# Performance work log

Hardware: AMD Instinct MI355X
Metric: run time of the kernel (lower is better)

The kernel has to match this reference:

```python
import jax, jax.numpy as jnp
import numpy as np

E, O, I = 8, 512, 1024  # num_experts, out_features, in_features
TOK_PER_EXPERT = 8192
T = E * TOK_PER_EXPERT  # total routed tokens


def setup_inputs() -> dict:
    key = jax.random.key(0)
    k1, k2 = jax.random.split(key)
    inputs = jax.random.normal(k1, (T, I), dtype=jnp.float32)
    # Learned per-expert weights, shape (E, O, I) as in GraniteMoeParallelExperts
    weight = jax.random.normal(k2, (E, O, I), dtype=jnp.float32) * (1.0 / np.sqrt(I))
    return {"inputs": inputs, "weight": weight, "expert_size": TOK_PER_EXPERT}


def reference(inputs, weight, expert_size):
    # inputs: [T, I] tokens sorted by expert; expert_size tokens per expert (static).
    # Equivalent to: split(inputs, expert_size) -> per-expert x @ W_e^T -> concat.
    e, o, i = weight.shape
    x = inputs.reshape(e, expert_size, i)          # [E, S, I]
    out = jnp.einsum('esi,eoi->eso', x, weight)    # grouped GEMM, [E, S, O]
    return out.reshape(e * expert_size, o)         # [T, O]
```

## Files before the change

kernel.cpp:

```cpp
#include <hip/hip_runtime.h>
#include <hip/hip_bf16.h>


#define NE 8
#define NO 512
#define NI 1024
#define NS 8192

#define BM 256
#define BN 256
#define BK 64
#define NT (NI / BK)

typedef __attribute__((ext_vector_type(4))) float f32x4;
typedef __attribute__((ext_vector_type(4))) short s16x4;
typedef __attribute__((ext_vector_type(8))) short s16x8;

__device__ __forceinline__ s16x4 cvt4(f32x4 a) {
    s16x4 r;
    r[0] = (short)__builtin_bit_cast(unsigned short, __float2bfloat16(a[0]));
    r[1] = (short)__builtin_bit_cast(unsigned short, __float2bfloat16(a[1]));
    r[2] = (short)__builtin_bit_cast(unsigned short, __float2bfloat16(a[2]));
    r[3] = (short)__builtin_bit_cast(unsigned short, __float2bfloat16(a[3]));
    return r;
}

__global__ __launch_bounds__(256)
void pack_w(const float* __restrict__ W, short* __restrict__ Wb) {
    size_t idx = (size_t)blockIdx.x * 256 + threadIdx.x;
    const float* src = W + idx * 8;
    f32x4 a = *(const f32x4*)src;
    f32x4 b = *(const f32x4*)(src + 4);
    s16x8 r;
    s16x4 lo = cvt4(a), hi = cvt4(b);
    r[0] = lo[0]; r[1] = lo[1]; r[2] = lo[2]; r[3] = lo[3];
    r[4] = hi[0]; r[5] = hi[1]; r[6] = hi[2]; r[7] = hi[3];
    *(s16x8*)(Wb + idx * 8) = r;
}

__global__ __launch_bounds__(512, 2)
void moe_gemm(const float* __restrict__ X,
              const short* __restrict__ Wb,
              float* __restrict__ Out) {
    int bid  = blockIdx.x;
    int swz  = (bid & 7) * 64 + (bid >> 3);
    int e    = swz >> 6;
    int rem  = swz & 63;
    int mblk = rem >> 1;
    int nblk = rem & 1;

    const float* Ap = X   + ((size_t)e * NS + (size_t)mblk * BM) * NI;
    const short* Bp = Wb  + ((size_t)e * NO + (size_t)nblk * BN) * NI;
    float*       Cp = Out + ((size_t)e * NS + (size_t)mblk * BM) * NO + nblk * BN;

    __shared__ short lA[2][BM * BK];
    __shared__ short lB[2][BN * BK];

    const int tid  = threadIdx.x;
    const int lane = tid & 63;
    const int wid  = tid >> 6;
    const int wm   = wid >> 2;
    const int wn   = wid & 3;
    const int l15  = lane & 15;
    const int lhi  = lane >> 4;

    f32x4 acc[8][4];
#pragma unroll
    for (int i = 0; i < 8; ++i)
#pragma unroll
        for (int j = 0; j < 4; ++j)
            acc[i][j] = (f32x4){0.f, 0.f, 0.f, 0.f};

    f32x4 ar[8];

#define AISSUE(kt)                                                             \
    do {                                                                       \
        _Pragma("unroll") for (int i = 0; i < 8; ++i) {                        \
            int u = tid + i * 512;                                             \
            ar[i] = *(const f32x4*)(Ap + (size_t)(u >> 4) * NI +               \
                                    (kt) * BK + (u & 15) * 4);                 \
        }                                                                      \
    } while (0)

#define AWRITE(buf)                                                            \
    do {                                                                       \
        _Pragma("unroll") for (int i = 0; i < 8; ++i) {                        \
            int u    = tid + i * 512;                                          \
            int row  = u >> 4;                                                 \
            int c4   = u & 15;                                                 \
            int phys = (c4 >> 1) ^ (row & 7);                                  \
            *(s16x4*)&lA[buf][row * 64 + phys * 8 + (c4 & 1) * 4] = cvt4(ar[i]); \
        }                                                                      \
    } while (0)

#define BSTAGE(kt, buf)                                                        \
    do {                                                                       \
        _Pragma("unroll") for (int j = 0; j < 4; ++j) {                        \
            int g    = (wid * 4 + j) * 64 + lane;                              \
            int row  = g >> 3;                                                 \
            int k16  = g & 7;                                                  \
            const short* gp = Bp + (size_t)row * NI + (kt) * BK +              \
                              ((k16 ^ (row & 7)) << 3);                        \
            short* lp = &lB[buf][(wid * 4 + j) * 512];                         \
            __builtin_amdgcn_global_load_lds(                                  \
                (const __attribute__((address_space(1))) void*)gp,             \
                (__attribute__((address_space(3))) void*)lp, 16, 0, 0);        \
        }                                                                      \
    } while (0)

#define COMPUTE(buf)                                                           \
    do {                                                                       \
        _Pragma("unroll") for (int kk = 0; kk < 2; ++kk) {                     \
            s16x8 af[8], bf_[4];                                               \
            _Pragma("unroll") for (int mi = 0; mi < 8; ++mi) {                 \
                int r    = wm * 128 + mi * 16 + l15;                           \
                int phys = (kk * 4 + lhi) ^ (r & 7);                           \
                af[mi]   = *(const s16x8*)&lA[buf][r * 64 + phys * 8];         \
            }                                                                  \
            _Pragma("unroll") for (int ni = 0; ni < 4; ++ni) {                 \
                int rb   = wn * 64 + ni * 16 + l15;                            \
                int phys = (kk * 4 + lhi) ^ (rb & 7);                          \
                bf_[ni]  = *(const s16x8*)&lB[buf][rb * 64 + phys * 8];        \
            }                                                                  \
            _Pragma("unroll") for (int mi = 0; mi < 8; ++mi)                   \
                _Pragma("unroll") for (int ni = 0; ni < 4; ++ni)               \
                    acc[mi][ni] = __builtin_amdgcn_mfma_f32_16x16x32_bf16(     \
                        af[mi], bf_[ni], acc[mi][ni], 0, 0, 0);                \
        }                                                                      \
    } while (0)

    AISSUE(0);
    BSTAGE(0, 0);

#pragma unroll 1
    for (int kt = 0; kt < NT; ++kt) {
        const int c = kt & 1;
        __builtin_amdgcn_s_barrier();
        asm volatile("s_waitcnt vmcnt(4)" ::: "memory");
        AWRITE(c);
        if (kt + 1 < NT) {
            AISSUE(kt + 1);
            BSTAGE(kt + 1, c ^ 1);
            asm volatile("s_waitcnt vmcnt(12)" ::: "memory");
        } else {
            asm volatile("s_waitcnt vmcnt(0)" ::: "memory");
        }
        asm volatile("s_waitcnt lgkmcnt(0)" ::: "memory");
        __builtin_amdgcn_s_barrier();
        COMPUTE(c);
    }

#pragma unroll
    for (int mi = 0; mi < 8; ++mi) {
#pragma unroll
        for (int rr = 0; rr < 4; ++rr) {
            int row   = wm * 128 + mi * 16 + lhi * 4 + rr;
            float* cp = Cp + (size_t)row * NO + wn * 64 + l15;
#pragma unroll
            for (int ni = 0; ni < 4; ++ni)
                cp[ni * 16] = acc[mi][ni][rr];
        }
    }
#undef AISSUE
#undef AWRITE
#undef BSTAGE
#undef COMPUTE
}

extern "C" void kernel_launch(void* const* d_in, const int* in_sizes, int n_in,
                              void* d_out, int out_size, void* d_ws, size_t ws_size,
                              hipStream_t stream) {
    const float* X = (const float*)d_in[0];
    const float* W = (const float*)d_in[1];
    float* Out     = (float*)d_out;
    short* Wb      = (short*)d_ws;

    hipLaunchKernelGGL(pack_w, dim3(2048), dim3(256), 0, stream, W, Wb);
    hipLaunchKernelGGL(moe_gemm, dim3(NE * (NS / BM) * (NO / BN)), dim3(512), 0,
                       stream, X, Wb, Out);
}
```

Baseline: 138.6 us.

## Restructure GEMM main loop into four interleaved phases with prefetch distance two

Splits each K-tile's compute into four phases of LDS reads plus MFMA, with barriers between them. The fp32 A loads and the bf16 conversion writes are spread across the phases, and A global loads are issued two tiles ahead. MFMA blocks run at raised priority via s_setprio. The occupancy hint drops to one 512-thread block per CU, giving more registers for the deeper prefetch and halved fragment arrays. The aim is to overlap global loads, LDS traffic and matrix math, at the cost of more barriers and lower occupancy.

Result: faster. 127.5 us (-8.0%).

```diff
diff --git a/kernel.cpp b/kernel.cpp
--- a/kernel.cpp
+++ b/kernel.cpp
@@ -38,7 +38,7 @@
     *(s16x8*)(Wb + idx * 8) = r;
 }
 
-__global__ __launch_bounds__(512, 2)
+__global__ __launch_bounds__(512, 1)
 void moe_gemm(const float* __restrict__ X,
               const short* __restrict__ Wb,
               float* __restrict__ Out) {
@@ -72,19 +72,20 @@
             acc[i][j] = (f32x4){0.f, 0.f, 0.f, 0.f};
 
     f32x4 ar[8];
-
-#define AISSUE(kt)                                                             \
-    do {                                                                       \
-        _Pragma("unroll") for (int i = 0; i < 8; ++i) {                        \
+    s16x8 af[4], bf_[4];
+
+#define AISSUE_H(kt, h)                                                        \
+    do {                                                                       \
+        _Pragma("unroll") for (int i = (h) * 4; i < (h) * 4 + 4; ++i) {        \
             int u = tid + i * 512;                                             \
             ar[i] = *(const f32x4*)(Ap + (size_t)(u >> 4) * NI +               \
                                     (kt) * BK + (u & 15) * 4);                 \
         }                                                                      \
     } while (0)
 
-#define AWRITE(buf)                                                            \
-    do {                                                                       \
-        _Pragma("unroll") for (int i = 0; i < 8; ++i) {                        \
+#define AWRITE_H(buf, h)                                                       \
+    do {                                                                       \
+        _Pragma("unroll") for (int i = (h) * 4; i < (h) * 4 + 4; ++i) {        \
             int u    = tid + i * 512;                                          \
             int row  = u >> 4;                                                 \
             int c4   = u & 15;                                                 \
@@ -108,46 +109,78 @@
         }                                                                      \
     } while (0)
 
-#define COMPUTE(buf)                                                           \
-    do {                                                                       \
-        _Pragma("unroll") for (int kk = 0; kk < 2; ++kk) {                     \
-            s16x8 af[8], bf_[4];                                               \
-            _Pragma("unroll") for (int mi = 0; mi < 8; ++mi) {                 \
-                int r    = wm * 128 + mi * 16 + l15;                           \
-                int phys = (kk * 4 + lhi) ^ (r & 7);                           \
-                af[mi]   = *(const s16x8*)&lA[buf][r * 64 + phys * 8];         \
-            }                                                                  \
-            _Pragma("unroll") for (int ni = 0; ni < 4; ++ni) {                 \
-                int rb   = wn * 64 + ni * 16 + l15;                            \
-                int phys = (kk * 4 + lhi) ^ (rb & 7);                          \
-                bf_[ni]  = *(const s16x8*)&lB[buf][rb * 64 + phys * 8];        \
-            }                                                                  \
-            _Pragma("unroll") for (int mi = 0; mi < 8; ++mi)                   \
-                _Pragma("unroll") for (int ni = 0; ni < 4; ++ni)               \
-                    acc[mi][ni] = __builtin_amdgcn_mfma_f32_16x16x32_bf16(     \
-                        af[mi], bf_[ni], acc[mi][ni], 0, 0, 0);                \
-        }                                                                      \
-    } while (0)
-
-    AISSUE(0);
+#define PH_READ_A(c, kk, mh)                                                   \
+    do {                                                                       \
+        _Pragma("unroll") for (int j = 0; j < 4; ++j) {                        \
+            int r    = wm * 128 + ((mh) * 4 + j) * 16 + l15;                   \
+            int phys = ((kk) * 4 + lhi) ^ (r & 7);                             \
+            af[j]    = *(const s16x8*)&lA[c][r * 64 + phys * 8];               \
+        }                                                                      \
+    } while (0)
+
+#define PH_READ_B(c, kk)                                                       \
+    do {                                                                       \
+        _Pragma("unroll") for (int ni = 0; ni < 4; ++ni) {                     \
+            int rb   = wn * 64 + ni * 16 + l15;                                \
+            int phys = ((kk) * 4 + lhi) ^ (rb & 7);                            \
+            bf_[ni]  = *(const s16x8*)&lB[c][rb * 64 + phys * 8];              \
+        }                                                                      \
+    } while (0)
+
+#define PH_MFMA(mh)                                                            \
+    do {                                                                       \
+        __builtin_amdgcn_s_setprio(1);                                         \
+        _Pragma("unroll") for (int j = 0; j < 4; ++j)                          \
+            _Pragma("unroll") for (int ni = 0; ni < 4; ++ni)                   \
+                acc[(mh) * 4 + j][ni] = __builtin_amdgcn_mfma_f32_16x16x32_bf16( \
+                    af[j], bf_[ni], acc[(mh) * 4 + j][ni], 0, 0, 0);           \
+        __builtin_amdgcn_s_setprio(0);                                         \
+    } while (0)
+
+#define BAR()   __builtin_amdgcn_s_barrier()
+#define LGKM0() asm volatile("s_waitcnt lgkmcnt(0)" ::: "memory")
+
+    AISSUE_H(0, 0); AISSUE_H(0, 1);
+    asm volatile("s_waitcnt vmcnt(0)" ::: "memory");
+    AWRITE_H(0, 0); AWRITE_H(0, 1);
     BSTAGE(0, 0);
+    AISSUE_H(1, 0); AISSUE_H(1, 1);
+    LGKM0();
+    asm volatile("s_waitcnt vmcnt(8)" ::: "memory");
+    BAR();
 
 #pragma unroll 1
     for (int kt = 0; kt < NT; ++kt) {
         const int c = kt & 1;
-        __builtin_amdgcn_s_barrier();
         asm volatile("s_waitcnt vmcnt(4)" ::: "memory");
-        AWRITE(c);
         if (kt + 1 < NT) {
-            AISSUE(kt + 1);
+            AWRITE_H(c ^ 1, 0);
             BSTAGE(kt + 1, c ^ 1);
-            asm volatile("s_waitcnt vmcnt(12)" ::: "memory");
-        } else {
-            asm volatile("s_waitcnt vmcnt(0)" ::: "memory");
         }
-        asm volatile("s_waitcnt lgkmcnt(0)" ::: "memory");
-        __builtin_amdgcn_s_barrier();
-        COMPUTE(c);
+        PH_READ_B(c, 0);
+        PH_READ_A(c, 0, 0);
+        BAR(); LGKM0();
+        PH_MFMA(0);
+        BAR();
+        asm volatile("s_waitcnt vmcnt(4)" ::: "memory");
+        if (kt + 1 < NT) AWRITE_H(c ^ 1, 1);
+        if (kt + 2 < NT) AISSUE_H(kt + 2, 0);
+        PH_READ_A(c, 0, 1);
+        BAR(); LGKM0();
+        PH_MFMA(1);
+        BAR();
+        if (kt + 2 < NT) AISSUE_H(kt + 2, 1);
+        PH_READ_B(c, 1);
+        PH_READ_A(c, 1, 0);
+        BAR(); LGKM0();
+        PH_MFMA(0);
+        BAR();
+        PH_READ_A(c, 1, 1);
+        if (kt + 2 < NT) { asm volatile("s_waitcnt vmcnt(8)" ::: "memory"); }
+        else             { asm volatile("s_waitcnt vmcnt(0)" ::: "memory"); }
+        BAR(); LGKM0();
+        PH_MFMA(1);
+        BAR();
     }
 
 #pragma unroll
@@ -161,10 +194,14 @@
                 cp[ni * 16] = acc[mi][ni][rr];
         }
     }
-#undef AISSUE
-#undef AWRITE
+#undef AISSUE_H
+#undef AWRITE_H
 #undef BSTAGE
-#undef COMPUTE
+#undef PH_READ_A
+#undef PH_READ_B
+#undef PH_MFMA
+#undef BAR
+#undef LGKM0
 }
 
 extern "C" void kernel_launch(void* const* d_in, const int* in_sizes, int n_in,
```
